# Performance work log

Hardware: AMD Instinct MI355X
Metric: run time of the kernel (lower is better)

Reference implementation:

```python
import jax, jax.numpy as jnp
import numpy as np

RADIUS = 0.2
NSAMPLE = 32
GROUPS = 4
EPS = 1e-5


def group_norm(x, gamma, beta):
    # x: [B, C, *spatial]; normalize per (batch, group) over channels-in-group + spatial
    B, C = x.shape[0], x.shape[1]
    rest = x.shape[2:]
    xr = x.reshape(B, GROUPS, -1)
    mean = xr.mean(-1, keepdims=True)
    var = xr.var(-1, keepdims=True)
    xr = (xr - mean) * jax.lax.rsqrt(var + EPS)
    x = xr.reshape((B, C) + rest)
    bshape = (1, C) + (1,) * len(rest)
    return x * gamma.reshape(bshape) + beta.reshape(bshape)


def ball_query(pos_t):
    # pos_t: [B, N, 3] -> idx [B, N, NSAMPLE] (query points == all points)
    N = pos_t.shape[1]
    sq = jnp.sum(pos_t * pos_t, axis=-1)  # [B, N]
    d = sq[:, :, None] + sq[:, None, :] - 2.0 * jnp.einsum('bnc,bmc->bnm', pos_t, pos_t)
    ar = jnp.arange(N, dtype=jnp.int32)
    gi = jnp.where(d > RADIUS * RADIUS, N, ar[None, None, :])  # [B, S, N]
    gi = jnp.sort(gi, axis=-1)[:, :, :NSAMPLE]  # ascending in-ball indices first
    first = gi[:, :, :1]
    gi = jnp.where(gi == N, first, gi)  # pad with first neighbor
    return gi


def setup_inputs() -> dict:
    key = jax.random.key(0)
    ks = jax.random.split(key, 6)
    B, C, N = 2, 64, 4096
    M = 4 * C  # mid channels
    return {
        'x': jax.random.normal(ks[0], (B, C, N), jnp.float32),
        'pos': jax.random.uniform(ks[1], (B, 3, N), jnp.float32),
        'w1': jax.random.normal(ks[2], (M, C), jnp.float32) * 0.05,
        'b1': jnp.zeros((M,), jnp.float32),
        'g1': jnp.ones((M,), jnp.float32),
        'be1': jnp.zeros((M,), jnp.float32),
        'wd': 1.0 + jax.random.normal(ks[3], (M,), jnp.float32) * 0.05,
        'gd': jnp.ones((M,), jnp.float32),
        'bed': jnp.zeros((M,), jnp.float32),
        'w2': jax.random.normal(ks[4], (C, M), jnp.float32) * 0.05,
        'b2': jnp.zeros((C,), jnp.float32),
        'g2': jnp.ones((C,), jnp.float32),
        'be2': jnp.zeros((C,), jnp.float32),
    }


def reference(x, pos, w1, b1, g1, be1, wd, gd, bed, w2, b2, g2, be2):
    # x: [B, C, N], pos: [B, 3, N]
    pos_t = jnp.transpose(pos, (0, 2, 1))  # [B, N, 3]
    idx = ball_query(pos_t)  # [B, N, K]

    # conv1 (1x1) -> GroupNorm -> GELU
    h = jnp.einsum('mc,bcn->bmn', w1, x) + b1[None, :, None]
    h = jax.nn.gelu(group_norm(h, g1, be1), approximate=False)  # [B, M, N]

    # gather neighbors: feats [B, N, M] indexed by idx [B, N, K]
    feats = jnp.transpose(h, (0, 2, 1))
    grouped = jax.vmap(lambda f, i: f[i])(feats, idx)  # [B, N, K, M]
    grouped = jnp.transpose(grouped, (0, 3, 1, 2))  # [B, M, N, K]

    # depthwise 1x1 conv (per-channel scale, no bias) -> GroupNorm -> max-pool over K -> GELU
    grouped = grouped * wd[None, :, None, None]
    grouped = group_norm(grouped, gd, bed)
    h2 = jax.nn.gelu(jnp.max(grouped, axis=-1), approximate=False)  # [B, M, N]

    # conv2 (1x1) -> GroupNorm -> residual
    out = jnp.einsum('cm,bmn->bcn', w2, h2) + b2[None, :, None]
    out = group_norm(out, g2, be2)
    return out + x
```

## Files before the change

kernel.cpp:

```cpp
#include <hip/hip_runtime.h>
#include <hip/hip_fp16.h>
#include <math.h>

#define BB 2
#define CC 64
#define NN 4096
#define MM 256
#define KK 32
#define GG 4
#define EPSF 1e-5f

__device__ __forceinline__ float gelu_exact(float x) {
    return 0.5f * x * (1.0f + erff(x * 0.70710678118654752f));
}

__device__ __forceinline__ unsigned pkmax(unsigned a, unsigned b) {
    unsigned d;
    asm("v_pk_max_f16 %0, %1, %2" : "=v"(d) : "v"(a), "v"(b));
    return d;
}
__device__ __forceinline__ unsigned pkmin(unsigned a, unsigned b) {
    unsigned d;
    asm("v_pk_min_f16 %0, %1, %2" : "=v"(d) : "v"(a), "v"(b));
    return d;
}
__device__ __forceinline__ unsigned selpair(unsigned mx, unsigned mn, float g0, float g1) {
    unsigned lo = (g0 >= 0.f) ? (mx & 0x0000FFFFu) : (mn & 0x0000FFFFu);
    unsigned hi = (g1 >= 0.f) ? (mx & 0xFFFF0000u) : (mn & 0xFFFF0000u);
    return lo | hi;
}
__device__ __forceinline__ float bcast_lane(float v, int lane) {
    return __int_as_float(__builtin_amdgcn_readlane(__float_as_int(v), lane));
}

__global__ void k_mlp1(const float* __restrict__ x, const float* __restrict__ w1,
                       const float* __restrict__ b1, __half* __restrict__ hH,
                       float2* __restrict__ Mp) {
    __shared__ float xs[64 * 128];
    __shared__ float w1t[64 * 32];
    __shared__ float r1[4], r2[4];

    int bx = blockIdx.x;
    int nt = bx & 31, mt = (bx >> 5) & 7, b = bx >> 8;
    int n0 = nt * 128, m0 = mt * 32;
    int t = threadIdx.x;

    {
        int nq = t & 31, ch = t >> 5;
        #pragma unroll
        for (int p = 0; p < 8; p++) {
            int c = p * 8 + ch;
            float4 v = *(const float4*)&x[((size_t)(b * CC + c)) * NN + n0 + nq * 4];
            *(float4*)&xs[c * 128 + nq * 4] = v;
        }
    }
    {
        #pragma unroll
        for (int p = 0; p < 2; p++) {
            int idx = p * 256 + t;
            int m = idx >> 4, cq = idx & 15;
            float4 v = *(const float4*)&w1[(m0 + m) * CC + cq * 4];
            w1t[(cq * 4 + 0) * 32 + m] = v.x;
            w1t[(cq * 4 + 1) * 32 + m] = v.y;
            w1t[(cq * 4 + 2) * 32 + m] = v.z;
            w1t[(cq * 4 + 3) * 32 + m] = v.w;
        }
    }
    __syncthreads();

    int nq = t & 31;
    int mseg = t >> 5;
    float o[4][4];
    #pragma unroll
    for (int i = 0; i < 4; i++)
        #pragma unroll
        for (int j = 0; j < 4; j++) o[i][j] = 0.f;

    for (int c = 0; c < 64; c++) {
        float4 xv = *(float4*)&xs[c * 128 + nq * 4];
        float4 wv = *(float4*)&w1t[c * 32 + mseg * 4];
        o[0][0] = fmaf(wv.x, xv.x, o[0][0]); o[0][1] = fmaf(wv.x, xv.y, o[0][1]);
        o[0][2] = fmaf(wv.x, xv.z, o[0][2]); o[0][3] = fmaf(wv.x, xv.w, o[0][3]);
        o[1][0] = fmaf(wv.y, xv.x, o[1][0]); o[1][1] = fmaf(wv.y, xv.y, o[1][1]);
        o[1][2] = fmaf(wv.y, xv.z, o[1][2]); o[1][3] = fmaf(wv.y, xv.w, o[1][3]);
        o[2][0] = fmaf(wv.z, xv.x, o[2][0]); o[2][1] = fmaf(wv.z, xv.y, o[2][1]);
        o[2][2] = fmaf(wv.z, xv.z, o[2][2]); o[2][3] = fmaf(wv.z, xv.w, o[2][3]);
        o[3][0] = fmaf(wv.w, xv.x, o[3][0]); o[3][1] = fmaf(wv.w, xv.y, o[3][1]);
        o[3][2] = fmaf(wv.w, xv.z, o[3][2]); o[3][3] = fmaf(wv.w, xv.w, o[3][3]);
    }

    float s1 = 0.f, s2 = 0.f;
    #pragma unroll
    for (int mi = 0; mi < 4; mi++) {
        int m = m0 + mseg * 4 + mi;
        float bv = b1[m];
        float4 r;
        r.x = o[mi][0] + bv; r.y = o[mi][1] + bv;
        r.z = o[mi][2] + bv; r.w = o[mi][3] + bv;
        __half2 hA = __float22half2_rn(make_float2(r.x, r.y));
        __half2 hB = __float22half2_rn(make_float2(r.z, r.w));
        uint2 st8;
        st8.x = *(unsigned*)&hA; st8.y = *(unsigned*)&hB;
        *(uint2*)((char*)hH + (((size_t)(b * MM + m)) * NN + n0 + nq * 4) * 2) = st8;
        s1 += r.x + r.y + r.z + r.w;
        s2 = fmaf(r.x, r.x, s2); s2 = fmaf(r.y, r.y, s2);
        s2 = fmaf(r.z, r.z, s2); s2 = fmaf(r.w, r.w, s2);
    }
    for (int off = 32; off; off >>= 1) {
        s1 += __shfl_down(s1, off, 64);
        s2 += __shfl_down(s2, off, 64);
    }
    int w = t >> 6, l = t & 63;
    if (l == 0) { r1[w] = s1; r2[w] = s2; }
    __syncthreads();
    if (t == 0) {
        Mp[bx] = make_float2(r1[0] + r1[1] + r1[2] + r1[3],
                             r2[0] + r2[1] + r2[2] + r2[3]);
    }
}

__global__ void k_gn1t_ballq(const __half* __restrict__ hH, const float* __restrict__ g1,
                             const float* __restrict__ be1, const float* __restrict__ wd,
                             const float2* __restrict__ Mp, __half* __restrict__ pH,
                             float* __restrict__ R,
                             const float* __restrict__ pos, int* __restrict__ idx) {
    __shared__ float tile[64 * 65];
    __shared__ float mv[2];
    int t = threadIdx.x;

    if (blockIdx.x < 512) {
        int id = blockIdx.x;
        int n0 = (id & 63) * 64;
        int g  = (id >> 6) & 3;
        int b  = id >> 8;
        int m0 = g * 64;

        if (t < 64) {
            float2 p2 = Mp[b * 256 + g * 64 + t];
            float s1 = p2.x, s2 = p2.y;
            for (int off = 32; off; off >>= 1) {
                s1 += __shfl_down(s1, off, 64);
                s2 += __shfl_down(s2, off, 64);
            }
            if (t == 0) {
                const double cnt = 64.0 * 4096.0;
                double md = (double)s1 / cnt;
                double vd = (double)s2 / cnt - md * md;
                mv[0] = (float)md;
                mv[1] = rsqrtf((float)vd + EPSF);
            }
        }
        __syncthreads();
        float mean = mv[0], rstd = mv[1];

        int nq = t & 15, mr = t >> 4;
        #pragma unroll
        for (int pp = 0; pp < 4; pp++) {
            int row = pp * 16 + mr;
            int m = m0 + row;
            float a = rstd * g1[m];
            float cc2 = be1[m] - mean * a;
            float wdm = wd[m];
            uint2 raw = *(const uint2*)((const char*)hH +
                         (((size_t)(b * MM + m)) * NN + n0 + nq * 4) * 2);
            float2 fa = __half22float2(*(__half2*)&raw.x);
            float2 fb = __half22float2(*(__half2*)&raw.y);
            tile[row * 65 + nq * 4 + 0] = gelu_exact(fmaf(fa.x, a, cc2)) * wdm;
            tile[row * 65 + nq * 4 + 1] = gelu_exact(fmaf(fa.y, a, cc2)) * wdm;
            tile[row * 65 + nq * 4 + 2] = gelu_exact(fmaf(fb.x, a, cc2)) * wdm;
            tile[row * 65 + nq * 4 + 3] = gelu_exact(fmaf(fb.y, a, cc2)) * wdm;
        }
        __syncthreads();
        #pragma unroll
        for (int pp = 0; pp < 4; pp++) {
            int id2 = pp * 256 + t;
            int nl = id2 >> 4, mq = id2 & 15;
            float a0 = tile[(mq * 4 + 0) * 65 + nl];
            float a1 = tile[(mq * 4 + 1) * 65 + nl];
            float a2 = tile[(mq * 4 + 2) * 65 + nl];
            float a3 = tile[(mq * 4 + 3) * 65 + nl];
            __half2 hA = __float22half2_rn(make_float2(a0, a1));
            __half2 hB = __float22half2_rn(make_float2(a2, a3));
            uint2 st8;
            st8.x = *(unsigned*)&hA; st8.y = *(unsigned*)&hB;
            *(uint2*)((char*)pH + ((((size_t)(b * NN) + n0 + nl)) << 9) + (m0 + mq * 4) * 2) = st8;
            float2 fa = __half22float2(hA);
            float2 fb = __half22float2(hB);
            float t1 = fa.x + fa.y + fb.x + fb.y;
            float t2 = fa.x * fa.x + fa.y * fa.y + fb.x * fb.x + fb.y * fb.y;
            #pragma unroll
            for (int off = 8; off; off >>= 1) {
                t1 += __shfl_down(t1, off, 16);
                t2 += __shfl_down(t2, off, 16);
            }
            if ((t & 15) == 0) {
                float* rr = &R[((size_t)(b * NN) + n0 + nl) * 8];
                rr[g]     = t1;
                rr[4 + g] = t2;
            }
        }
    } else {
        int bx = blockIdx.x - 512;
        int wid  = bx * 4 + (threadIdx.x >> 6);
        int lane = threadIdx.x & 63;
        int b = wid >> 12;
        int n = wid & 4095;
        const float* px = pos + b * 3 * NN;
        const float* py = px + NN;
        const float* pz = py + NN;
        float qx = px[n], qy = py[n], qz = pz[n];
        float qsq = qx*qx + qy*qy + qz*qz;
        int* row = idx + (b * NN + n) * KK;

        int found = 0;
        int first = -1;
        const float R2 = 0.04f;
        for (int m0 = 0; m0 < NN && found < KK; m0 += 64) {
            int m = m0 + lane;
            float ax = px[m], ay = py[m], az = pz[m];
            float msq = ax*ax + ay*ay + az*az;
            float dot = qx*ax + qy*ay + qz*az;
            float d = qsq + msq - 2.0f * dot;
            bool hit = !(d > R2);
            unsigned long long mask = __ballot(hit);
            if (first < 0 && mask) first = m0 + (__ffsll((long long)mask) - 1);
            unsigned long long lt = (lane == 0) ? 0ULL : (mask & ((1ULL << lane) - 1ULL));
            int posh = __popcll(lt);
            if (hit && (found + posh) < KK) row[found + posh] = m;
            found += __popcll(mask);
            if (found > KK) found = KK;
        }
        if (lane < KK && lane >= found) row[lane] = first;
    }
}

__global__ __launch_bounds__(256)
void k_qgather_gstats(const __half* __restrict__ pH, const int* __restrict__ idx,
                      const float* __restrict__ R, const float* __restrict__ gd,
                      __half* __restrict__ pselH, float* __restrict__ Gp) {
    __shared__ float sAcc[8][8];
    int t = threadIdx.x;

    if (blockIdx.x < 2048) {
        int q = blockIdx.x;
        int b = ((q & 7) < 4) ? 0 : 1;
        int local = (q >> 3) * 4 + (q & 3);
        int w = t >> 6, l = t & 63;
        int gn = b * NN + local * 4 + w;

        int hh = l >> 5, cl = l & 31;
        int myidx = idx[gn * KK + cl];
        const char* pb = (const char*)(pH + (size_t)b * NN * 256);
        int laneoff = cl * 16;

        unsigned vmax0 = 0xFC00FC00u, vmax1 = 0xFC00FC00u, vmax2 = 0xFC00FC00u, vmax3 = 0xFC00FC00u;
        unsigned vmin0 = 0x7C007C00u, vmin1 = 0x7C007C00u, vmin2 = 0x7C007C00u, vmin3 = 0x7C007C00u;

        #pragma unroll
        for (int kb = 0; kb < 4; kb++) {
            int jj[4];
            #pragma unroll
            for (int u = 0; u < 4; u++) {
                int k = kb * 4 + u;
                int ja = __shfl(myidx, 2 * k, 64);
                int jb = __shfl(myidx, 2 * k + 1, 64);
                jj[u] = hh ? jb : ja;
            }
            uint4 r[4];
            #pragma unroll
            for (int u = 0; u < 4; u++)
                r[u] = *(const uint4*)(pb + (((size_t)jj[u]) << 9) + laneoff);
            #pragma unroll
            for (int u = 0; u < 4; u++) {
                vmax0 = pkmax(vmax0, r[u].x); vmin0 = pkmin(vmin0, r[u].x);
                vmax1 = pkmax(vmax1, r[u].y); vmin1 = pkmin(vmin1, r[u].y);
                vmax2 = pkmax(vmax2, r[u].z); vmin2 = pkmin(vmin2, r[u].z);
                vmax3 = pkmax(vmax3, r[u].w); vmin3 = pkmin(vmin3, r[u].w);
            }
        }
        vmax0 = pkmax(vmax0, (unsigned)__shfl_xor((int)vmax0, 32, 64));
        vmax1 = pkmax(vmax1, (unsigned)__shfl_xor((int)vmax1, 32, 64));
        vmax2 = pkmax(vmax2, (unsigned)__shfl_xor((int)vmax2, 32, 64));
        vmax3 = pkmax(vmax3, (unsigned)__shfl_xor((int)vmax3, 32, 64));
        vmin0 = pkmin(vmin0, (unsigned)__shfl_xor((int)vmin0, 32, 64));
        vmin1 = pkmin(vmin1, (unsigned)__shfl_xor((int)vmin1, 32, 64));
        vmin2 = pkmin(vmin2, (unsigned)__shfl_xor((int)vmin2, 32, 64));
        vmin3 = pkmin(vmin3, (unsigned)__shfl_xor((int)vmin3, 32, 64));

        if (hh == 0) {
            const float4* g4 = (const float4*)gd;
            float4 gA = g4[cl * 2], gB = g4[cl * 2 + 1];
            uint4 o4;
            o4.x = selpair(vmax0, vmin0, gA.x, gA.y);
            o4.y = selpair(vmax1, vmin1, gA.z, gA.w);
            o4.z = selpair(vmax2, vmin2, gB.x, gB.y);
            o4.w = selpair(vmax3, vmin3, gB.z, gB.w);
            *(uint4*)((char*)pselH + (((size_t)gn) << 9) + laneoff) = o4;
        }
    } else {
        int bid = blockIdx.x - 2048;
        int hw = t >> 5, cl = t & 31;
        int pbase = bid * 32;
        int b = pbase >> 12;
        float s[8];
        #pragma unroll
        for (int c = 0; c < 8; c++) s[c] = 0.f;
        #pragma unroll
        for (int it = 0; it < 4; it++) {
            int pt = pbase + it * 8 + hw;
            int j = idx[pt * KK + cl];
            const float* rr = &R[((size_t)(b * NN) + j) * 8];
            float4 ra = *(const float4*)rr;
            float4 rb = *(const float4*)(rr + 4);
            s[0] += ra.x; s[1] += ra.y; s[2] += ra.z; s[3] += ra.w;
            s[4] += rb.x; s[5] += rb.y; s[6] += rb.z; s[7] += rb.w;
        }
        #pragma unroll
        for (int off = 16; off; off >>= 1) {
            #pragma unroll
            for (int c = 0; c < 8; c++) s[c] += __shfl_down(s[c], off, 32);
        }
        if (cl == 0) {
            #pragma unroll
            for (int c = 0; c < 8; c++) sAcc[hw][c] = s[c];
        }
        __syncthreads();
        if (t < 8) {
            float v = 0.f;
            #pragma unroll
            for (int k = 0; k < 8; k++) v += sAcc[k][t];
            Gp[bid * 8 + t] = v;
        }
    }
}

__global__ __launch_bounds__(256, 4)
void k_mlp2(const __half* __restrict__ pselH, const float* __restrict__ Gp,
            const float* __restrict__ w2, const float* __restrict__ b2,
            const float* __restrict__ gd, const float* __restrict__ bed,
            float* __restrict__ oraw, float* __restrict__ Op) {
    __shared__ float w2s[64 * 257];
    __shared__ float sw[4][8];
    __shared__ float sA[4][4], sB[4][4];

    int t = threadIdx.x;
    int w = t >> 6, l = t & 63;
    int q = blockIdx.x;
    int b = ((q & 7) < 4) ? 0 : 1;
    int local = (q >> 3) * 4 + (q & 3);
    int n0 = local * 16 + w * 4;

    #pragma unroll
    for (int p = 0; p < 16; p++) {
        int i = p * 256 + t;
        int c = i >> 6, mq = i & 63;
        float4 v = ((const float4*)w2)[i];
        float* dst = &w2s[c * 257 + mq * 4];
        dst[0] = v.x; dst[1] = v.y; dst[2] = v.z; dst[3] = v.w;
    }

    {
        float s[8] = {0.f, 0.f, 0.f, 0.f, 0.f, 0.f, 0.f, 0.f};
        if (t < 128) {
            const float4* gp = (const float4*)(Gp + ((size_t)(b * 128 + t)) * 8);
            float4 ra = gp[0], rb = gp[1];
            s[0] = ra.x; s[1] = ra.y; s[2] = ra.z; s[3] = ra.w;
            s[4] = rb.x; s[5] = rb.y; s[6] = rb.z; s[7] = rb.w;
        }
        #pragma unroll
        for (int off = 32; off; off >>= 1) {
            #pragma unroll
            for (int c = 0; c < 8; c++) s[c] += __shfl_down(s[c], off, 64);
        }
        if (l == 0) {
            #pragma unroll
            for (int c = 0; c < 8; c++) sw[w][c] = s[c];
        }
    }
    __syncthreads();

    int g = l >> 4;
    double s1 = (double)sw[0][g] + sw[1][g] + sw[2][g] + sw[3][g];
    double s2 = (double)sw[0][4 + g] + sw[1][4 + g] + sw[2][4 + g] + sw[3][4 + g];
    const double cnt2 = 64.0 * 4096.0 * 32.0;
    double m_ = s1 / cnt2;
    double v_ = s2 / cnt2 - m_ * m_;
    float mean = (float)m_;
    float rstd = rsqrtf((float)v_ + EPSF);
    float4 gd4  = ((const float4*)gd)[l];
    float4 bed4 = ((const float4*)bed)[l];
    float ax = rstd * gd4.x, ay = rstd * gd4.y, az = rstd * gd4.z, aw = rstd * gd4.w;
    float cx = bed4.x - mean * ax, cy = bed4.y - mean * ay;
    float cz = bed4.z - mean * az, cw = bed4.w - mean * aw;

    float4 h2r[4];
    #pragma unroll
    for (int j = 0; j < 4; j++) {
        uint2 raw = *(const uint2*)((const char*)pselH +
                     ((((size_t)(b * NN)) + n0 + j) << 9) + l * 8);
        float2 fa = __half22float2(*(__half2*)&raw.x);
        float2 fb = __half22float2(*(__half2*)&raw.y);
        h2r[j].x = gelu_exact(fmaf(fa.x, ax, cx));
        h2r[j].y = gelu_exact(fmaf(fa.y, ay, cy));
        h2r[j].z = gelu_exact(fmaf(fb.x, az, cz));
        h2r[j].w = gelu_exact(fmaf(fb.y, aw, cw));
    }

    const float* w2l = &w2s[l * 257];
    float acc[4] = {0.f, 0.f, 0.f, 0.f};
    #pragma unroll 8
    for (int mq = 0; mq < 64; mq++) {
        float w0  = w2l[4 * mq + 0];
        float w1_ = w2l[4 * mq + 1];
        float w2_ = w2l[4 * mq + 2];
        float w3_ = w2l[4 * mq + 3];
        #pragma unroll
        for (int j = 0; j < 4; j++) {
            acc[j] = fmaf(w0,  bcast_lane(h2r[j].x, mq), acc[j]);
            acc[j] = fmaf(w1_, bcast_lane(h2r[j].y, mq), acc[j]);
            acc[j] = fmaf(w2_, bcast_lane(h2r[j].z, mq), acc[j]);
            acc[j] = fmaf(w3_, bcast_lane(h2r[j].w, mq), acc[j]);
        }
    }

    float bias = b2[l];
    float so1 = 0.f, so2 = 0.f;
    #pragma unroll
    for (int j = 0; j < 4; j++) {
        acc[j] += bias;
        so1 += acc[j];
        so2 = fmaf(acc[j], acc[j], so2);
    }
    *(float4*)&oraw[((size_t)(b * CC) + l) * NN + n0] =
        make_float4(acc[0], acc[1], acc[2], acc[3]);

    so1 += __shfl_down(so1, 8, 16); so2 += __shfl_down(so2, 8, 16);
    so1 += __shfl_down(so1, 4, 16); so2 += __shfl_down(so2, 4, 16);
    so1 += __shfl_down(so1, 2, 16); so2 += __shfl_down(so2, 2, 16);
    so1 += __shfl_down(so1, 1, 16); so2 += __shfl_down(so2, 1, 16);
    if ((l & 15) == 0) { sA[w][l >> 4] = so1; sB[w][l >> 4] = so2; }
    __syncthreads();
    if (t < 8) {
        int is2 = t >> 2, gg = t & 3;
        float v = is2 ? (sB[0][gg] + sB[1][gg] + sB[2][gg] + sB[3][gg])
                      : (sA[0][gg] + sA[1][gg] + sA[2][gg] + sA[3][gg]);
        Op[(b * 256 + local) * 8 + t] = v;
    }
}

__global__ void k_final(const float* __restrict__ oraw, const float* __restrict__ x,
                        const float* __restrict__ g2, const float* __restrict__ be2,
                        const float* __restrict__ Op, float* __restrict__ out) {
    __shared__ float fw[4][8];
    int t = threadIdx.x;
    int i4 = blockIdx.x * 256 + t;
    int base = i4 * 4;
    int b = base >> 18;

    {
        const float4* rp = (const float4*)(Op + ((size_t)(b * 256 + t)) * 8);
        float4 ra = rp[0], rb = rp[1];
        float s[8] = {ra.x, ra.y, ra.z, ra.w, rb.x, rb.y, rb.z, rb.w};
        #pragma unroll
        for (int off = 32; off; off >>= 1) {
            #pragma unroll
            for (int c = 0; c < 8; c++) s[c] += __shfl_down(s[c], off, 64);
        }
        if ((t & 63) == 0) {
            #pragma unroll
            for (int c = 0; c < 8; c++) fw[t >> 6][c] = s[c];
        }
    }
    __syncthreads();

    int c = (base >> 12) & 63;
    int g = c >> 4;
    double s1 = (double)fw[0][g] + fw[1][g] + fw[2][g] + fw[3][g];
    double s2 = (double)fw[0][4 + g] + fw[1][4 + g] + fw[2][4 + g] + fw[3][4 + g];
    const double cnt = 16.0 * 4096.0;
    double mean_d = s1 / cnt;
    double var_d  = s2 / cnt - mean_d * mean_d;
    float mean = (float)mean_d;
    float rstd = rsqrtf((float)var_d + EPSF);
    float sc = rstd * g2[c];
    float ad = be2[c] - mean * sc;
    float4 o = ((const float4*)oraw)[i4];
    float4 xv = ((const float4*)x)[i4];
    float4 r;
    r.x = fmaf(o.x, sc, ad) + xv.x;
    r.y = fmaf(o.y, sc, ad) + xv.y;
    r.z = fmaf(o.z, sc, ad) + xv.z;
    r.w = fmaf(o.w, sc, ad) + xv.w;
    ((float4*)out)[i4] = r;
}

extern "C" void kernel_launch(void* const* d_in, const int* in_sizes, int n_in,
                              void* d_out, int out_size, void* d_ws, size_t ws_size,
                              hipStream_t stream) {
    const float* x   = (const float*)d_in[0];
    const float* pos = (const float*)d_in[1];
    const float* w1  = (const float*)d_in[2];
    const float* b1  = (const float*)d_in[3];
    const float* g1  = (const float*)d_in[4];
    const float* be1 = (const float*)d_in[5];
    const float* wd  = (const float*)d_in[6];
    const float* gd  = (const float*)d_in[7];
    const float* bed = (const float*)d_in[8];
    const float* w2  = (const float*)d_in[9];
    const float* b2  = (const float*)d_in[10];
    const float* g2  = (const float*)d_in[11];
    const float* be2 = (const float*)d_in[12];
    float* out = (float*)d_out;

    char* wsb = (char*)d_ws;
    __half* hH    = (__half*)wsb;
    __half* pH    = (__half*)(wsb + 8388608);
    __half* pselH = (__half*)(wsb + 12582912);
    float*  oraw  = (float*)(wsb + 16777216);
    int*    idx   = (int*)(wsb + 18874368);
    float*  R     = (float*)(wsb + 19922944);
    float2* Mp    = (float2*)(wsb + 20185088);
    float*  Gp    = (float*)(wsb + 20189184);
    float*  Op    = (float*)(wsb + 20197376);

    k_mlp1<<<512, 256, 0, stream>>>(x, w1, b1, hH, Mp);
    k_gn1t_ballq<<<2560, 256, 0, stream>>>(hH, g1, be1, wd, Mp, pH, R, pos, idx);
    k_qgather_gstats<<<2304, 256, 0, stream>>>(pH, idx, R, gd, pselH, Gp);
    k_mlp2<<<512, 256, 0, stream>>>(pselH, Gp, w2, b2, gd, bed, oraw, Op);
    k_final<<<512, 256, 0, stream>>>(oraw, x, g2, be2, Op, out);
}
```

Before: 145.3 us.

## Fuse neighbor gather/max-select into conv2 kernel via shared memory

Moves the per-point neighbor gather with packed-half max/min selection out of the separate gather kernel and into the conv2 kernel. The selected values go to shared memory instead of a global pselH buffer, so one intermediate write and read pass disappears. The group-stats part becomes its own small kernel. In exchange, the conv2 kernel does each wave's gather serially over 4 points with fewer blocks (512 vs 2048 gather blocks). Its occupancy hint drops to 2, which may reduce latency hiding for the random gathers.

```diff
diff --git a/kernel.cpp b/kernel.cpp
--- a/kernel.cpp
+++ b/kernel.cpp
@@ -234,112 +234,53 @@
     }
 }
 
-__global__ __launch_bounds__(256)
-void k_qgather_gstats(const __half* __restrict__ pH, const int* __restrict__ idx,
-                      const float* __restrict__ R, const float* __restrict__ gd,
-                      __half* __restrict__ pselH, float* __restrict__ Gp) {
+__global__ void k_gstats(const int* __restrict__ idx, const float* __restrict__ R,
+                         float* __restrict__ Gp) {
     __shared__ float sAcc[8][8];
     int t = threadIdx.x;
-
-    if (blockIdx.x < 2048) {
-        int q = blockIdx.x;
-        int b = ((q & 7) < 4) ? 0 : 1;
-        int local = (q >> 3) * 4 + (q & 3);
-        int w = t >> 6, l = t & 63;
-        int gn = b * NN + local * 4 + w;
-
-        int hh = l >> 5, cl = l & 31;
-        int myidx = idx[gn * KK + cl];
-        const char* pb = (const char*)(pH + (size_t)b * NN * 256);
-        int laneoff = cl * 16;
-
-        unsigned vmax0 = 0xFC00FC00u, vmax1 = 0xFC00FC00u, vmax2 = 0xFC00FC00u, vmax3 = 0xFC00FC00u;
-        unsigned vmin0 = 0x7C007C00u, vmin1 = 0x7C007C00u, vmin2 = 0x7C007C00u, vmin3 = 0x7C007C00u;
-
-        #pragma unroll
-        for (int kb = 0; kb < 4; kb++) {
-            int jj[4];
-            #pragma unroll
-            for (int u = 0; u < 4; u++) {
-                int k = kb * 4 + u;
-                int ja = __shfl(myidx, 2 * k, 64);
-                int jb = __shfl(myidx, 2 * k + 1, 64);
-                jj[u] = hh ? jb : ja;
-            }
-            uint4 r[4];
-            #pragma unroll
-            for (int u = 0; u < 4; u++)
-                r[u] = *(const uint4*)(pb + (((size_t)jj[u]) << 9) + laneoff);
-            #pragma unroll
-            for (int u = 0; u < 4; u++) {
-                vmax0 = pkmax(vmax0, r[u].x); vmin0 = pkmin(vmin0, r[u].x);
-                vmax1 = pkmax(vmax1, r[u].y); vmin1 = pkmin(vmin1, r[u].y);
-                vmax2 = pkmax(vmax2, r[u].z); vmin2 = pkmin(vmin2, r[u].z);
-                vmax3 = pkmax(vmax3, r[u].w); vmin3 = pkmin(vmin3, r[u].w);
-            }
-        }
-        vmax0 = pkmax(vmax0, (unsigned)__shfl_xor((int)vmax0, 32, 64));
-        vmax1 = pkmax(vmax1, (unsigned)__shfl_xor((int)vmax1, 32, 64));
-        vmax2 = pkmax(vmax2, (unsigned)__shfl_xor((int)vmax2, 32, 64));
-        vmax3 = pkmax(vmax3, (unsigned)__shfl_xor((int)vmax3, 32, 64));
-        vmin0 = pkmin(vmin0, (unsigned)__shfl_xor((int)vmin0, 32, 64));
-        vmin1 = pkmin(vmin1, (unsigned)__shfl_xor((int)vmin1, 32, 64));
-        vmin2 = pkmin(vmin2, (unsigned)__shfl_xor((int)vmin2, 32, 64));
-        vmin3 = pkmin(vmin3, (unsigned)__shfl_xor((int)vmin3, 32, 64));
-
-        if (hh == 0) {
-            const float4* g4 = (const float4*)gd;
-            float4 gA = g4[cl * 2], gB = g4[cl * 2 + 1];
-            uint4 o4;
-            o4.x = selpair(vmax0, vmin0, gA.x, gA.y);
-            o4.y = selpair(vmax1, vmin1, gA.z, gA.w);
-            o4.z = selpair(vmax2, vmin2, gB.x, gB.y);
-            o4.w = selpair(vmax3, vmin3, gB.z, gB.w);
-            *(uint4*)((char*)pselH + (((size_t)gn) << 9) + laneoff) = o4;
-        }
-    } else {
-        int bid = blockIdx.x - 2048;
-        int hw = t >> 5, cl = t & 31;
-        int pbase = bid * 32;
-        int b = pbase >> 12;
-        float s[8];
-        #pragma unroll
-        for (int c = 0; c < 8; c++) s[c] = 0.f;
-        #pragma unroll
-        for (int it = 0; it < 4; it++) {
-            int pt = pbase + it * 8 + hw;
-            int j = idx[pt * KK + cl];
-            const float* rr = &R[((size_t)(b * NN) + j) * 8];
-            float4 ra = *(const float4*)rr;
-            float4 rb = *(const float4*)(rr + 4);
-            s[0] += ra.x; s[1] += ra.y; s[2] += ra.z; s[3] += ra.w;
-            s[4] += rb.x; s[5] += rb.y; s[6] += rb.z; s[7] += rb.w;
-        }
-        #pragma unroll
-        for (int off = 16; off; off >>= 1) {
-            #pragma unroll
-            for (int c = 0; c < 8; c++) s[c] += __shfl_down(s[c], off, 32);
-        }
-        if (cl == 0) {
-            #pragma unroll
-            for (int c = 0; c < 8; c++) sAcc[hw][c] = s[c];
-        }
-        __syncthreads();
-        if (t < 8) {
-            float v = 0.f;
-            #pragma unroll
-            for (int k = 0; k < 8; k++) v += sAcc[k][t];
-            Gp[bid * 8 + t] = v;
-        }
-    }
-}
-
-__global__ __launch_bounds__(256, 4)
-void k_mlp2(const __half* __restrict__ pselH, const float* __restrict__ Gp,
-            const float* __restrict__ w2, const float* __restrict__ b2,
-            const float* __restrict__ gd, const float* __restrict__ bed,
-            float* __restrict__ oraw, float* __restrict__ Op) {
+    int bid = blockIdx.x;
+    int hw = t >> 5, cl = t & 31;
+    int pbase = bid * 32;
+    int b = pbase >> 12;
+    float s[8];
+    #pragma unroll
+    for (int c = 0; c < 8; c++) s[c] = 0.f;
+    #pragma unroll
+    for (int it = 0; it < 4; it++) {
+        int pt = pbase + it * 8 + hw;
+        int j = idx[pt * KK + cl];
+        const float* rr = &R[((size_t)(b * NN) + j) * 8];
+        float4 ra = *(const float4*)rr;
+        float4 rb = *(const float4*)(rr + 4);
+        s[0] += ra.x; s[1] += ra.y; s[2] += ra.z; s[3] += ra.w;
+        s[4] += rb.x; s[5] += rb.y; s[6] += rb.z; s[7] += rb.w;
+    }
+    #pragma unroll
+    for (int off = 16; off; off >>= 1) {
+        #pragma unroll
+        for (int c = 0; c < 8; c++) s[c] += __shfl_down(s[c], off, 32);
+    }
+    if (cl == 0) {
+        #pragma unroll
+        for (int c = 0; c < 8; c++) sAcc[hw][c] = s[c];
+    }
+    __syncthreads();
+    if (t < 8) {
+        float v = 0.f;
+        #pragma unroll
+        for (int k = 0; k < 8; k++) v += sAcc[k][t];
+        Gp[bid * 8 + t] = v;
+    }
+}
+
+__global__ __launch_bounds__(256, 2)
+void k_mlp2g(const __half* __restrict__ pH, const int* __restrict__ idx,
+             const float* __restrict__ Gp, const float* __restrict__ w2,
+             const float* __restrict__ b2, const float* __restrict__ gd,
+             const float* __restrict__ bed, float* __restrict__ oraw,
+             float* __restrict__ Op) {
     __shared__ float w2s[64 * 257];
+    __shared__ uint4 phs4[4][4][32];
     __shared__ float sw[4][8];
     __shared__ float sA[4][4], sB[4][4];
 
@@ -393,11 +334,64 @@
     float cx = bed4.x - mean * ax, cy = bed4.y - mean * ay;
     float cz = bed4.z - mean * az, cw = bed4.w - mean * aw;
 
+    {
+        int hh = l >> 5, cl = l & 31;
+        const char* pb = (const char*)(pH + (size_t)b * NN * 256);
+        int laneoff = cl * 16;
+        const float4* g4 = (const float4*)gd;
+        float4 gA = g4[cl * 2], gB = g4[cl * 2 + 1];
+        #pragma unroll
+        for (int p = 0; p < 4; p++) {
+            int myidx = idx[((size_t)(b * NN) + n0 + p) * KK + cl];
+            unsigned vmax0 = 0xFC00FC00u, vmax1 = 0xFC00FC00u, vmax2 = 0xFC00FC00u, vmax3 = 0xFC00FC00u;
+            unsigned vmin0 = 0x7C007C00u, vmin1 = 0x7C007C00u, vmin2 = 0x7C007C00u, vmin3 = 0x7C007C00u;
+            #pragma unroll
+            for (int kb = 0; kb < 4; kb++) {
+                int jj[4];
+                #pragma unroll
+                for (int u = 0; u < 4; u++) {
+                    int k = kb * 4 + u;
+                    int ja = __shfl(myidx, 2 * k, 64);
+                    int jb = __shfl(myidx, 2 * k + 1, 64);
+                    jj[u] = hh ? jb : ja;
+                }
+                uint4 r[4];
+                #pragma unroll
+                for (int u = 0; u < 4; u++)
+                    r[u] = *(const uint4*)(pb + (((size_t)jj[u]) << 9) + laneoff);
+                #pragma unroll
+                for (int u = 0; u < 4; u++) {
+                    vmax0 = pkmax(vmax0, r[u].x); vmin0 = pkmin(vmin0, r[u].x);
+                    vmax1 = pkmax(vmax1, r[u].y); vmin1 = pkmin(vmin1, r[u].y);
+                    vmax2 = pkmax(vmax2, r[u].z); vmin2 = pkmin(vmin2, r[u].z);
+                    vmax3 = pkmax(vmax3, r[u].w); vmin3 = pkmin(vmin3, r[u].w);
+                }
+            }
+            vmax0 = pkmax(vmax0, (unsigned)__shfl_xor((int)vmax0, 32, 64));
+            vmax1 = pkmax(vmax1, (unsigned)__shfl_xor((int)vmax1, 32, 64));
+            vmax2 = pkmax(vmax2, (unsigned)__shfl_xor((int)vmax2, 32, 64));
+            vmax3 = pkmax(vmax3, (unsigned)__shfl_xor((int)vmax3, 32, 64));
+            vmin0 = pkmin(vmin0, (unsigned)__shfl_xor((int)vmin0, 32, 64));
+            vmin1 = pkmin(vmin1, (unsigned)__shfl_xor((int)vmin1, 32, 64));
+            vmin2 = pkmin(vmin2, (unsigned)__shfl_xor((int)vmin2, 32, 64));
+            vmin3 = pkmin(vmin3, (unsigned)__shfl_xor((int)vmin3, 32, 64));
+
+            if (hh == 0) {
+                uint4 o4;
+                o4.x = selpair(vmax0, vmin0, gA.x, gA.y);
+                o4.y = selpair(vmax1, vmin1, gA.z, gA.w);
+                o4.z = selpair(vmax2, vmin2, gB.x, gB.y);
+                o4.w = selpair(vmax3, vmin3, gB.z, gB.w);
+                phs4[w][p][cl] = o4;
+            }
+        }
+    }
+
     float4 h2r[4];
     #pragma unroll
     for (int j = 0; j < 4; j++) {
-        uint2 raw = *(const uint2*)((const char*)pselH +
-                     ((((size_t)(b * NN)) + n0 + j) << 9) + l * 8);
+        const uint2* pr = (const uint2*)&phs4[w][j][0];
+        uint2 raw = pr[l];
         float2 fa = __half22float2(*(__half2*)&raw.x);
         float2 fb = __half22float2(*(__half2*)&raw.y);
         h2r[j].x = gelu_exact(fmaf(fa.x, ax, cx));
@@ -515,7 +509,6 @@
     char* wsb = (char*)d_ws;
     __half* hH    = (__half*)wsb;
     __half* pH    = (__half*)(wsb + 8388608);
-    __half* pselH = (__half*)(wsb + 12582912);
     float*  oraw  = (float*)(wsb + 16777216);
     int*    idx   = (int*)(wsb + 18874368);
     float*  R     = (float*)(wsb + 19922944);
@@ -525,7 +518,7 @@
 
     k_mlp1<<<512, 256, 0, stream>>>(x, w1, b1, hH, Mp);
     k_gn1t_ballq<<<2560, 256, 0, stream>>>(hH, g1, be1, wd, Mp, pH, R, pos, idx);
-    k_qgather_gstats<<<2304, 256, 0, stream>>>(pH, idx, R, gd, pselH, Gp);
-    k_mlp2<<<512, 256, 0, stream>>>(pselH, Gp, w2, b2, gd, bed, oraw, Op);
+    k_gstats<<<256, 256, 0, stream>>>(idx, R, Gp);
+    k_mlp2g<<<512, 256, 0, stream>>>(pH, idx, Gp, w2, b2, gd, bed, oraw, Op);
     k_final<<<512, 256, 0, stream>>>(oraw, x, g2, be2, Op, out);
 }
```

After: 146.1 us. Within noise of the previous version (+0.5%).
